# Optimization experiments

Hardware: AMD Instinct MI355X
Metric: run time of the kernel (lower is better)

## Reference

```python
import jax, jax.numpy as jnp
import numpy as np
import math

D_MODEL = 1024
NUM_HEADS = 16
B, L = 2, 2048
# scale_level=0, patch_time_span=1 -> effective_stride=1
PERIODS = (1.0, 30.0)
WEIGHTS = (0.8, 0.4)
SIGMAS = (0.5, 2.0)


def setup_inputs() -> dict:
    key = jax.random.key(0)
    ks = jax.random.split(key, 10)
    s = 1.0 / math.sqrt(D_MODEL)
    inp = {
        "x": jax.random.normal(ks[0], (B, L, D_MODEL), dtype=jnp.float32),
        "Wq": jax.random.normal(ks[1], (D_MODEL, D_MODEL), dtype=jnp.float32) * s,
        "bq": jax.random.normal(ks[2], (D_MODEL,), dtype=jnp.float32) * 0.01,
        "Wk": jax.random.normal(ks[3], (D_MODEL, D_MODEL), dtype=jnp.float32) * s,
        "bk": jax.random.normal(ks[4], (D_MODEL,), dtype=jnp.float32) * 0.01,
        "Wv": jax.random.normal(ks[5], (D_MODEL, D_MODEL), dtype=jnp.float32) * s,
        "bv": jax.random.normal(ks[6], (D_MODEL,), dtype=jnp.float32) * 0.01,
        "Wo": jax.random.normal(ks[7], (D_MODEL, D_MODEL), dtype=jnp.float32) * s,
        "bo": jax.random.normal(ks[8], (D_MODEL,), dtype=jnp.float32) * 0.01,
        "prior_lambda": jnp.asarray(2.0, dtype=jnp.float32),
    }
    return inp


def _gaussian_mask(length):
    idx = jnp.arange(length, dtype=jnp.float32)
    delta = jnp.abs(idx[:, None] - idx[None, :])  # [L, L]
    mask = jnp.zeros_like(delta)
    for p, w, sigma in zip(PERIODS, WEIGHTS, SIGMAS):
        if p < 0.2:
            continue
        mask = mask + w * jnp.exp(-((delta - p) ** 2) / (2.0 * sigma ** 2))
    return mask


def reference(x, Wq, bq, Wk, bk, Wv, bv, Wo, bo, prior_lambda):
    Bx, Lx, D = x.shape
    H = NUM_HEADS
    hd = D // H

    def split_heads(t):  # [B, L, D] -> [B, H, L, hd]
        return t.reshape(Bx, Lx, H, hd).transpose(0, 2, 1, 3)

    Q = split_heads(x @ Wq.T + bq)
    K = split_heads(x @ Wk.T + bk)
    V = split_heads(x @ Wv.T + bv)

    scores = jnp.einsum("bhqd,bhkd->bhqk", Q, K) / math.sqrt(hd)
    scores = scores + prior_lambda * _gaussian_mask(Lx)[None, None, :, :]
    attn = jax.nn.softmax(scores, axis=-1)
    out = jnp.einsum("bhqk,bhkd->bhqd", attn, V)
    out = out.transpose(0, 2, 1, 3).reshape(Bx, Lx, D)
    return out @ Wo.T + bo
```

## Files before the change

### kernel.cpp

```cpp
#include <hip/hip_runtime.h>

#define D_MODEL 1024
#define SEQ_L   2048
#define NHEADS  16
#define HDIM    64
#define NROWS   4096

typedef __attribute__((ext_vector_type(8))) short short8;
typedef __attribute__((ext_vector_type(4))) float floatx4;
typedef __attribute__((ext_vector_type(4))) unsigned short ushort4v;
typedef unsigned short ushort;

static __device__ __forceinline__ ushort f2bf(float f) {
    unsigned int u = __float_as_uint(f);
    u += 0x7FFFu + ((u >> 16) & 1u);
    return (ushort)(u >> 16);
}

static __device__ __forceinline__ floatx4 mfma16(short8 a, short8 b, floatx4 c) {
    return __builtin_amdgcn_mfma_f32_16x16x32_bf16(a, b, c, 0, 0, 0);
}

static __device__ __forceinline__ void store8bf(ushort* dst, float4 a, float4 b) {
    uint4 pk;
    pk.x = (unsigned)f2bf(a.x) | ((unsigned)f2bf(a.y) << 16);
    pk.y = (unsigned)f2bf(a.z) | ((unsigned)f2bf(a.w) << 16);
    pk.z = (unsigned)f2bf(b.x) | ((unsigned)f2bf(b.y) << 16);
    pk.w = (unsigned)f2bf(b.z) | ((unsigned)f2bf(b.w) << 16);
    *(uint4*)dst = pk;
}

static __device__ __forceinline__ void gll16(const ushort* g, ushort* l) {
    __builtin_amdgcn_global_load_lds(
        (const __attribute__((address_space(1))) unsigned int*)(const unsigned int*)g,
        (__attribute__((address_space(3))) unsigned int*)(unsigned int*)l,
        16, 0, 0);
}

__global__ __launch_bounds__(256) void convert_bf16(
    const float* __restrict__ x,
    const float* __restrict__ wq, const float* __restrict__ wk,
    const float* __restrict__ wv, const float* __restrict__ wo,
    ushort* __restrict__ xb, ushort* __restrict__ wb3, ushort* __restrict__ wob)
{
    const int seg = blockIdx.y;
    const float* src;
    ushort* dst;
    int n;
    if      (seg == 0) { src = x;  dst = xb;                n = 4194304; }
    else if (seg == 1) { src = wq; dst = wb3;               n = 1048576; }
    else if (seg == 2) { src = wk; dst = wb3 + 1048576;     n = 1048576; }
    else if (seg == 3) { src = wv; dst = wb3 + 2097152;     n = 1048576; }
    else               { src = wo; dst = wob;               n = 1048576; }
    const int i = (blockIdx.x * 256 + threadIdx.x) * 8;
    if (i >= n) return;
    float4 a = *(const float4*)(src + i);
    float4 b = *(const float4*)(src + i + 4);
    store8bf(dst + i, a, b);
}

__global__ __launch_bounds__(256) void gemm_qkv(
    const ushort* __restrict__ A, const ushort* __restrict__ B,
    const float* __restrict__ bq, const float* __restrict__ bk,
    const float* __restrict__ bv,
    ushort* __restrict__ Qo, ushort* __restrict__ Ko, ushort* __restrict__ Vo)
{
    __shared__ ushort As[128 * 32];
    __shared__ ushort Bs[128 * 32];

    const int tid  = threadIdx.x;
    const int w    = tid >> 6;
    const int lane = tid & 63;
    const int l15  = lane & 15;
    const int quad = lane >> 4;
    const int wm   = w & 1;
    const int wn   = w >> 1;

    const int bm = blockIdx.y * 128;
    const int bn = blockIdx.x * 128;

    const int r0 = w * 16 + (lane >> 2);
    const int r1 = r0 + 64;
    const int c_ = lane & 3;
    const int g0 = c_ ^ ((r0 >> 1) & 3);
    const int g1 = c_ ^ ((r1 >> 1) & 3);

    const ushort* a0p = A + (size_t)(bm + r0) * 1024 + g0 * 8;
    const ushort* a1p = A + (size_t)(bm + r1) * 1024 + g1 * 8;
    const ushort* b0p = B + (size_t)(bn + r0) * 1024 + g0 * 8;
    const ushort* b1p = B + (size_t)(bn + r1) * 1024 + g1 * 8;
    ushort* lA0 = &As[r0 * 32 + c_ * 8];
    ushort* lA1 = &As[r1 * 32 + c_ * 8];
    ushort* lB0 = &Bs[r0 * 32 + c_ * 8];
    ushort* lB1 = &Bs[r1 * 32 + c_ * 8];

    const int cA = (quad ^ ((l15 >> 1) & 3)) * 8;

    floatx4 acc[4][4];
#pragma unroll
    for (int i = 0; i < 4; i++)
#pragma unroll
        for (int j = 0; j < 4; j++) acc[i][j] = (floatx4){0.f, 0.f, 0.f, 0.f};

    for (int k0 = 0; k0 < 1024; k0 += 32) {
        __syncthreads();
        gll16(a0p + k0, lA0);
        gll16(a1p + k0, lA1);
        gll16(b0p + k0, lB0);
        gll16(b1p + k0, lB1);
        __syncthreads();

        short8 af[4], bf[4];
#pragma unroll
        for (int mi = 0; mi < 4; mi++)
            af[mi] = *(const short8*)&As[(wm * 64 + mi * 16 + l15) * 32 + cA];
#pragma unroll
        for (int ni = 0; ni < 4; ni++)
            bf[ni] = *(const short8*)&Bs[(wn * 64 + ni * 16 + l15) * 32 + cA];
#pragma unroll
        for (int mi = 0; mi < 4; mi++)
#pragma unroll
            for (int ni = 0; ni < 4; ni++)
                acc[mi][ni] = mfma16(af[mi], bf[ni], acc[mi][ni]);
    }

#pragma unroll
    for (int ni = 0; ni < 4; ni++) {
        const int col = bn + wn * 64 + ni * 16 + l15;
        const int z = col >> 10;
        const int within = col & 1023;
        const int h  = within >> 6;
        const int hd = within & 63;
        const float* bias = (z == 0) ? bq : (z == 1) ? bk : bv;
        const float bvl = bias[within];
        if (z == 2) {
#pragma unroll
            for (int mi = 0; mi < 4; mi++) {
                const int row = bm + wm * 64 + mi * 16 + quad * 4;
                const int bb = row >> 11, li = row & 2047;
                ushort4v pk;
#pragma unroll
                for (int r = 0; r < 4; r++) pk[r] = f2bf(acc[mi][ni][r] + bvl);
                *(ushort4v*)(Vo + ((size_t)(bb * NHEADS + h) * HDIM + hd) * SEQ_L + li) = pk;
            }
        } else {
            const float scale = (z == 0) ? 0.125f : 1.0f;
            ushort* outp = (z == 0) ? Qo : Ko;
#pragma unroll
            for (int mi = 0; mi < 4; mi++) {
#pragma unroll
                for (int r = 0; r < 4; r++) {
                    const int row = bm + wm * 64 + mi * 16 + quad * 4 + r;
                    const int bb = row >> 11, li = row & 2047;
                    outp[((size_t)(bb * NHEADS + h) * SEQ_L + li) * HDIM + hd] =
                        f2bf((acc[mi][ni][r] + bvl) * scale);
                }
            }
        }
    }
}

__global__ __launch_bounds__(256) void attn(
    const ushort* __restrict__ Q,
    const ushort* __restrict__ K,
    const ushort* __restrict__ Vt,
    const float* __restrict__ lam,
    ushort* __restrict__ O)
{
    __shared__ float mtab[128];
    __shared__ ushort Ks[64][72];
    __shared__ ushort Vts[64][72];
    __shared__ ushort Ps[4][16][68];

    const int tid  = threadIdx.x;
    const int wave = tid >> 6;
    const int lane = tid & 63;
    const int l15  = lane & 15;
    const int quad = lane >> 4;

    const int qb = blockIdx.x;
    const int h  = blockIdx.y;
    const int bz = blockIdx.z;
    const int bh = bz * NHEADS + h;
    const int q0 = qb * 64;

    const float lambda = *lam;
    if (tid < 128) {
        float d  = (float)tid;
        float e1 = (d - 1.f) * (d - 1.f);
        float e2 = (d - 30.f) * (d - 30.f);
        mtab[tid] = lambda * (0.8f * __expf(-2.0f * e1) + 0.4f * __expf(-0.125f * e2));
    }

    const ushort* qp =
        Q + ((size_t)bh * SEQ_L + q0 + wave * 16 + l15) * HDIM + quad * 8;
    short8 qf[2];
    qf[0] = *(const short8*)qp;
    qf[1] = *(const short8*)(qp + 32);

    floatx4 o[4];
#pragma unroll
    for (int i = 0; i < 4; i++) o[i] = (floatx4){0.f, 0.f, 0.f, 0.f};
    float lrun[4] = {0.f, 0.f, 0.f, 0.f};

    const int sr  = tid >> 2;
    const int sc2 = (tid & 3) * 16;

    const ushort* kbase = K  + ((size_t)bh * SEQ_L) * HDIM;
    const ushort* vbase = Vt + ((size_t)bh * HDIM) * SEQ_L;

    for (int j = 0; j < SEQ_L / 64; j++) {
        const ushort* kp = kbase + (size_t)(j * 64 + sr) * HDIM + sc2;
        uint4 kv0 = *(const uint4*)kp;
        uint4 kv1 = *(const uint4*)(kp + 8);
        const ushort* vp = vbase + (size_t)sr * SEQ_L + j * 64 + sc2;
        uint4 vv0 = *(const uint4*)vp;
        uint4 vv1 = *(const uint4*)(vp + 8);
        __syncthreads();
        *(uint4*)&Ks[sr][sc2]      = kv0;
        *(uint4*)&Ks[sr][sc2 + 8]  = kv1;
        *(uint4*)&Vts[sr][sc2]     = vv0;
        *(uint4*)&Vts[sr][sc2 + 8] = vv1;
        __syncthreads();

        floatx4 s[4];
#pragma unroll
        for (int i = 0; i < 4; i++) s[i] = (floatx4){0.f, 0.f, 0.f, 0.f};
#pragma unroll
        for (int kk = 0; kk < 2; kk++) {
#pragma unroll
            for (int nt = 0; nt < 4; nt++) {
                short8 bfrag = *(const short8*)&Ks[nt * 16 + l15][kk * 32 + quad * 8];
                s[nt] = mfma16(qf[kk], bfrag, s[nt]);
            }
        }

        const int dj = j - qb;
        if (dj >= -1 && dj <= 1) {
            const int qrow0 = q0 + wave * 16 + quad * 4;
#pragma unroll
            for (int nt = 0; nt < 4; nt++) {
                const int kg = j * 64 + nt * 16 + l15;
#pragma unroll
                for (int r = 0; r < 4; r++) {
                    int dq = qrow0 + r - kg;
                    int ad = dq < 0 ? -dq : dq;
                    s[nt][r] += mtab[ad];
                }
            }
        }

#pragma unroll
        for (int nt = 0; nt < 4; nt++) {
#pragma unroll
            for (int r = 0; r < 4; r++) {
                float p = __expf(s[nt][r]);
                lrun[r] += p;
                Ps[wave][quad * 4 + r][nt * 16 + l15] = f2bf(p);
            }
        }
        __syncthreads();

#pragma unroll
        for (int kk = 0; kk < 2; kk++) {
            short8 pa = *(const short8*)&Ps[wave][l15][kk * 32 + quad * 8];
#pragma unroll
            for (int nt = 0; nt < 4; nt++) {
                short8 vb = *(const short8*)&Vts[nt * 16 + l15][kk * 32 + quad * 8];
                o[nt] = mfma16(pa, vb, o[nt]);
            }
        }
    }

    float linv[4];
#pragma unroll
    for (int r = 0; r < 4; r++) {
        float s_ = lrun[r];
#pragma unroll
        for (int off = 1; off < 16; off <<= 1) s_ += __shfl_xor(s_, off, 16);
        linv[r] = 1.f / s_;
    }
#pragma unroll
    for (int nt = 0; nt < 4; nt++) {
        const int hd = nt * 16 + l15;
#pragma unroll
        for (int r = 0; r < 4; r++) {
            const int qg = q0 + wave * 16 + quad * 4 + r;
            O[((size_t)bz * SEQ_L + qg) * D_MODEL + h * HDIM + hd] =
                f2bf(o[nt][r] * linv[r]);
        }
    }
}

__global__ __launch_bounds__(256) void gemm_out(
    const ushort* __restrict__ A, const ushort* __restrict__ B,
    const float* __restrict__ bo, float* __restrict__ out)
{
    __shared__ ushort As[64 * 32];
    __shared__ ushort Bs[128 * 32];

    const int tid  = threadIdx.x;
    const int w    = tid >> 6;
    const int lane = tid & 63;
    const int l15  = lane & 15;
    const int quad = lane >> 4;

    const int bm = blockIdx.y * 64;
    const int bn = blockIdx.x * 128;

    const int r0 = w * 16 + (lane >> 2);
    const int r1 = r0 + 64;
    const int c_ = lane & 3;
    const int g0 = c_ ^ ((r0 >> 1) & 3);
    const int g1 = c_ ^ ((r1 >> 1) & 3);

    const ushort* a0p = A + (size_t)(bm + r0) * 1024 + g0 * 8;
    const ushort* b0p = B + (size_t)(bn + r0) * 1024 + g0 * 8;
    const ushort* b1p = B + (size_t)(bn + r1) * 1024 + g1 * 8;
    ushort* lA0 = &As[r0 * 32 + c_ * 8];
    ushort* lB0 = &Bs[r0 * 32 + c_ * 8];
    ushort* lB1 = &Bs[r1 * 32 + c_ * 8];

    const int cA = (quad ^ ((l15 >> 1) & 3)) * 8;

    floatx4 acc[4][2];
#pragma unroll
    for (int i = 0; i < 4; i++)
#pragma unroll
        for (int j = 0; j < 2; j++) acc[i][j] = (floatx4){0.f, 0.f, 0.f, 0.f};

    for (int k0 = 0; k0 < 1024; k0 += 32) {
        __syncthreads();
        gll16(a0p + k0, lA0);
        gll16(b0p + k0, lB0);
        gll16(b1p + k0, lB1);
        __syncthreads();

        short8 af[4], bf[2];
#pragma unroll
        for (int mi = 0; mi < 4; mi++)
            af[mi] = *(const short8*)&As[(mi * 16 + l15) * 32 + cA];
#pragma unroll
        for (int ni = 0; ni < 2; ni++)
            bf[ni] = *(const short8*)&Bs[(w * 32 + ni * 16 + l15) * 32 + cA];
#pragma unroll
        for (int mi = 0; mi < 4; mi++)
#pragma unroll
            for (int ni = 0; ni < 2; ni++)
                acc[mi][ni] = mfma16(af[mi], bf[ni], acc[mi][ni]);
    }

#pragma unroll
    for (int ni = 0; ni < 2; ni++) {
        const int col = bn + w * 32 + ni * 16 + l15;
        const float bvl = bo[col];
#pragma unroll
        for (int mi = 0; mi < 4; mi++) {
#pragma unroll
            for (int r = 0; r < 4; r++) {
                const int row = bm + mi * 16 + quad * 4 + r;
                out[(size_t)row * 1024 + col] = acc[mi][ni][r] + bvl;
            }
        }
    }
}

extern "C" void kernel_launch(void* const* d_in, const int* in_sizes, int n_in,
                              void* d_out, int out_size, void* d_ws, size_t ws_size,
                              hipStream_t stream)
{
    const float* x   = (const float*)d_in[0];
    const float* Wq  = (const float*)d_in[1];
    const float* bq  = (const float*)d_in[2];
    const float* Wk  = (const float*)d_in[3];
    const float* bk  = (const float*)d_in[4];
    const float* Wv  = (const float*)d_in[5];
    const float* bv  = (const float*)d_in[6];
    const float* Wo  = (const float*)d_in[7];
    const float* bo  = (const float*)d_in[8];
    const float* lam = (const float*)d_in[9];
    float* out = (float*)d_out;

    const size_t NELEM = (size_t)NROWS * D_MODEL;
    ushort* Qw  = (ushort*)d_ws;
    ushort* Kw  = Qw + NELEM;
    ushort* Vw  = Kw + NELEM;
    ushort* XA  = Vw + NELEM;
    ushort* Wb3 = XA + NELEM;
    ushort* Wob = Wb3 + 3 * 1024 * 1024;

    dim3 gc(2048, 5);
    convert_bf16<<<gc, 256, 0, stream>>>(x, Wq, Wk, Wv, Wo, XA, Wb3, Wob);

    dim3 g1(3072 / 128, NROWS / 128);
    gemm_qkv<<<g1, 256, 0, stream>>>(XA, Wb3, bq, bk, bv, Qw, Kw, Vw);

    dim3 g2(SEQ_L / 64, NHEADS, 2);
    attn<<<g2, 256, 0, stream>>>(Qw, Kw, Vw, lam, XA);

    dim3 g3(1024 / 128, NROWS / 64);
    gemm_out<<<g3, 256, 0, stream>>>(XA, Wob, bo, out);
}
```

Before: 232.9 us.

## Double-buffer K/V via direct-to-LDS loads and keep P in registers

The attention kernel now double-buffers K and V tiles in LDS using global_load_lds with an XOR swizzle, prefetching the next tile while computing the current one. It computes S transposed (K as the A operand) so the probability tile lands in a register layout usable directly as the B operand of a 16x16x16 bf16 MFMA. This removes the P shared-memory round trip and one barrier per iteration. The row sum is accumulated from the rounded bf16 values and the output is written with vectorized 4-element stores. It uses more LDS and relies on the async load being complete at the next barrier.

```diff
diff --git a/kernel.cpp b/kernel.cpp
--- a/kernel.cpp
+++ b/kernel.cpp
@@ -7,6 +7,7 @@
 #define NROWS   4096
 
 typedef __attribute__((ext_vector_type(8))) short short8;
+typedef __attribute__((ext_vector_type(4))) short short4v;
 typedef __attribute__((ext_vector_type(4))) float floatx4;
 typedef __attribute__((ext_vector_type(4))) unsigned short ushort4v;
 typedef unsigned short ushort;
@@ -19,6 +20,10 @@
 
 static __device__ __forceinline__ floatx4 mfma16(short8 a, short8 b, floatx4 c) {
     return __builtin_amdgcn_mfma_f32_16x16x32_bf16(a, b, c, 0, 0, 0);
+}
+
+static __device__ __forceinline__ floatx4 mfma16k16(short4v a, short4v b, floatx4 c) {
+    return __builtin_amdgcn_mfma_f32_16x16x16bf16_1k(a, b, c, 0, 0, 0);
 }
 
 static __device__ __forceinline__ void store8bf(ushort* dst, float4 a, float4 b) {
@@ -168,9 +173,8 @@
     ushort* __restrict__ O)
 {
     __shared__ float mtab[128];
-    __shared__ ushort Ks[64][72];
-    __shared__ ushort Vts[64][72];
-    __shared__ ushort Ps[4][16][68];
+    __shared__ ushort Ks[2][64 * 64];
+    __shared__ ushort Vts[2][64 * 64];
 
     const int tid  = threadIdx.x;
     const int wave = tid >> 6;
@@ -198,30 +202,41 @@
     qf[0] = *(const short8*)qp;
     qf[1] = *(const short8*)(qp + 32);
 
-    floatx4 o[4];
-#pragma unroll
-    for (int i = 0; i < 4; i++) o[i] = (floatx4){0.f, 0.f, 0.f, 0.f};
-    float lrun[4] = {0.f, 0.f, 0.f, 0.f};
-
-    const int sr  = tid >> 2;
-    const int sc2 = (tid & 3) * 16;
-
     const ushort* kbase = K  + ((size_t)bh * SEQ_L) * HDIM;
     const ushort* vbase = Vt + ((size_t)bh * HDIM) * SEQ_L;
 
+    const int cid0 = tid, cid1 = 256 + tid;
+    const int row0 = cid0 >> 3, row1 = cid1 >> 3;
+    const int cl0  = (cid0 & 7) ^ (row0 & 7);
+    const int cl1  = (cid1 & 7) ^ (row1 & 7);
+    const ushort* kg0 = kbase + (size_t)row0 * HDIM + cl0 * 8;
+    const ushort* kg1 = kbase + (size_t)row1 * HDIM + cl1 * 8;
+    const ushort* vg0 = vbase + (size_t)row0 * SEQ_L + cl0 * 8;
+    const ushort* vg1 = vbase + (size_t)row1 * SEQ_L + cl1 * 8;
+
+    floatx4 o[4];
+#pragma unroll
+    for (int i = 0; i < 4; i++) o[i] = (floatx4){0.f, 0.f, 0.f, 0.f};
+    float lrun = 0.f;
+
+    gll16(kg0, &Ks[0][cid0 * 8]);
+    gll16(kg1, &Ks[0][cid1 * 8]);
+    gll16(vg0, &Vts[0][cid0 * 8]);
+    gll16(vg1, &Vts[0][cid1 * 8]);
+
+    const int xo = l15 & 7;
+
     for (int j = 0; j < SEQ_L / 64; j++) {
-        const ushort* kp = kbase + (size_t)(j * 64 + sr) * HDIM + sc2;
-        uint4 kv0 = *(const uint4*)kp;
-        uint4 kv1 = *(const uint4*)(kp + 8);
-        const ushort* vp = vbase + (size_t)sr * SEQ_L + j * 64 + sc2;
-        uint4 vv0 = *(const uint4*)vp;
-        uint4 vv1 = *(const uint4*)(vp + 8);
+        const int cur = j & 1;
         __syncthreads();
-        *(uint4*)&Ks[sr][sc2]      = kv0;
-        *(uint4*)&Ks[sr][sc2 + 8]  = kv1;
-        *(uint4*)&Vts[sr][sc2]     = vv0;
-        *(uint4*)&Vts[sr][sc2 + 8] = vv1;
-        __syncthreads();
+        if (j + 1 < SEQ_L / 64) {
+            const int nxt = cur ^ 1;
+            const int koff = (j + 1) * 64;
+            gll16(kg0 + (size_t)koff * HDIM, &Ks[nxt][cid0 * 8]);
+            gll16(kg1 + (size_t)koff * HDIM, &Ks[nxt][cid1 * 8]);
+            gll16(vg0 + koff, &Vts[nxt][cid0 * 8]);
+            gll16(vg1 + koff, &Vts[nxt][cid1 * 8]);
+        }
 
         floatx4 s[4];
 #pragma unroll
@@ -230,65 +245,70 @@
         for (int kk = 0; kk < 2; kk++) {
 #pragma unroll
             for (int nt = 0; nt < 4; nt++) {
-                short8 bfrag = *(const short8*)&Ks[nt * 16 + l15][kk * 32 + quad * 8];
-                s[nt] = mfma16(qf[kk], bfrag, s[nt]);
+                const int slot = (kk * 4 + quad) ^ xo;
+                short8 kf = *(const short8*)&Ks[cur][(nt * 16 + l15) * 64 + slot * 8];
+                s[nt] = mfma16(kf, qf[kk], s[nt]);
             }
         }
 
         const int dj = j - qb;
         if (dj >= -1 && dj <= 1) {
-            const int qrow0 = q0 + wave * 16 + quad * 4;
+            const int qg = q0 + wave * 16 + l15;
 #pragma unroll
             for (int nt = 0; nt < 4; nt++) {
-                const int kg = j * 64 + nt * 16 + l15;
+                const int kg = j * 64 + nt * 16 + quad * 4;
 #pragma unroll
                 for (int r = 0; r < 4; r++) {
-                    int dq = qrow0 + r - kg;
+                    int dq = qg - (kg + r);
                     int ad = dq < 0 ? -dq : dq;
                     s[nt][r] += mtab[ad];
                 }
             }
         }
 
+        short4v pb[4];
 #pragma unroll
         for (int nt = 0; nt < 4; nt++) {
+            unsigned ur[4];
 #pragma unroll
             for (int r = 0; r < 4; r++) {
                 float p = __expf(s[nt][r]);
-                lrun[r] += p;
-                Ps[wave][quad * 4 + r][nt * 16 + l15] = f2bf(p);
-            }
-        }
-        __syncthreads();
-
-#pragma unroll
-        for (int kk = 0; kk < 2; kk++) {
-            short8 pa = *(const short8*)&Ps[wave][l15][kk * 32 + quad * 8];
+                unsigned u = __float_as_uint(p);
+                u += 0x7FFFu + ((u >> 16) & 1u);
+                ur[r] = u;
+                lrun += __uint_as_float(u & 0xFFFF0000u);
+            }
+            uint2 pk;
+            pk.x = __builtin_amdgcn_perm(ur[1], ur[0], 0x07060302u);
+            pk.y = __builtin_amdgcn_perm(ur[3], ur[2], 0x07060302u);
+            pb[nt] = __builtin_bit_cast(short4v, pk);
+        }
+
+#pragma unroll
+        for (int kc = 0; kc < 4; kc++) {
 #pragma unroll
             for (int nt = 0; nt < 4; nt++) {
-                short8 vb = *(const short8*)&Vts[nt * 16 + l15][kk * 32 + quad * 8];
-                o[nt] = mfma16(pa, vb, o[nt]);
-            }
-        }
-    }
-
-    float linv[4];
-#pragma unroll
-    for (int r = 0; r < 4; r++) {
-        float s_ = lrun[r];
-#pragma unroll
-        for (int off = 1; off < 16; off <<= 1) s_ += __shfl_xor(s_, off, 16);
-        linv[r] = 1.f / s_;
-    }
+                const int slot = (2 * kc + (quad >> 1)) ^ xo;
+                short4v vf = *(const short4v*)
+                    &Vts[cur][(nt * 16 + l15) * 64 + slot * 8 + (quad & 1) * 4];
+                o[nt] = mfma16k16(vf, pb[kc], o[nt]);
+            }
+        }
+    }
+
+    float s_ = lrun;
+    s_ += __shfl_xor(s_, 16);
+    s_ += __shfl_xor(s_, 32);
+    const float linv = 1.f / s_;
+
+    const int qg = q0 + wave * 16 + l15;
+    ushort* obase = O + ((size_t)bz * SEQ_L + qg) * D_MODEL + h * HDIM;
 #pragma unroll
     for (int nt = 0; nt < 4; nt++) {
-        const int hd = nt * 16 + l15;
-#pragma unroll
-        for (int r = 0; r < 4; r++) {
-            const int qg = q0 + wave * 16 + quad * 4 + r;
-            O[((size_t)bz * SEQ_L + qg) * D_MODEL + h * HDIM + hd] =
-                f2bf(o[nt][r] * linv[r]);
-        }
+        ushort4v pk;
+#pragma unroll
+        for (int r = 0; r < 4; r++) pk[r] = f2bf(o[nt][r] * linv);
+        *(ushort4v*)(obase + nt * 16 + quad * 4) = pk;
     }
 }
 
```

New measurement: 224.4 us. 1.04x faster.
